# Performance work log

Hardware: AMD Instinct MI355X
Metric: run time of the kernel (lower is better)

Reference implementation:

```python
import jax, jax.numpy as jnp
import numpy as np

B, S, H = 1, 2048, 4096
NH, NKV, HD = 32, 8, 128
GROUP = 128
NEG = jnp.float32(-1e9)


def setup_inputs() -> dict:
    key = jax.random.key(0)
    ks = jax.random.split(key, 13)
    inp = {"hidden_states": jax.random.normal(ks[0], (B, S, H), dtype=jnp.float32)}

    def qparams(k1, k2, k3, out_dim, in_dim):
        qw = jax.random.randint(k1, (out_dim, in_dim), 0, 16, dtype=jnp.int32)
        sc = jax.random.uniform(k2, (out_dim, in_dim // GROUP), dtype=jnp.float32) * 0.02 + 0.001
        zp = jax.random.randint(k3, (out_dim, in_dim // GROUP), 0, 16, dtype=jnp.int32)
        return qw, sc, zp

    inp["q_qw"], inp["q_sc"], inp["q_zp"] = qparams(ks[1], ks[2], ks[3], NH * HD, H)
    inp["k_qw"], inp["k_sc"], inp["k_zp"] = qparams(ks[4], ks[5], ks[6], NKV * HD, H)
    inp["v_qw"], inp["v_sc"], inp["v_zp"] = qparams(ks[7], ks[8], ks[9], NKV * HD, H)
    inp["o_qw"], inp["o_sc"], inp["o_zp"] = qparams(ks[10], ks[11], ks[12], NH * HD, H)
    return inp


def dequant(qw, sc, zp):
    # W4A16 groupwise dequant: w = (q - zero_point) * scale, group along input dim
    out_dim, in_dim = qw.shape
    g = in_dim // sc.shape[1]
    w = (qw.reshape(out_dim, -1, g) - zp[:, :, None]).astype(jnp.float32) * sc[:, :, None]
    return w.reshape(out_dim, in_dim)


def reference(hidden_states, q_qw, q_sc, q_zp, k_qw, k_sc, k_zp,
              v_qw, v_sc, v_zp, o_qw, o_sc, o_zp):
    x = hidden_states  # [B, S, H]
    grp = NH // NKV  # GQA groups = 4

    q = jnp.einsum('bsh,oh->bso', x, dequant(q_qw, q_sc, q_zp))
    k = jnp.einsum('bsh,oh->bso', x, dequant(k_qw, k_sc, k_zp))
    v = jnp.einsum('bsh,oh->bso', x, dequant(v_qw, v_sc, v_zp))

    # [B, NKV, grp, S, HD] for q; [B, NKV, S, HD] for k, v (avoid repeat_kv materialization)
    q = q.reshape(B, S, NKV, grp, HD).transpose(0, 2, 3, 1, 4)
    k = k.reshape(B, S, NKV, HD).transpose(0, 2, 1, 3)
    v = v.reshape(B, S, NKV, HD).transpose(0, 2, 1, 3)

    scale = 1.0 / jnp.sqrt(jnp.float32(HD))
    scores = jnp.einsum('bngqd,bnkd->bngqk', q, k) * scale  # [B,NKV,grp,S,S]
    causal = jnp.tril(jnp.ones((S, S), dtype=bool))
    scores = jnp.where(causal[None, None, None], scores, NEG)
    probs = jax.nn.softmax(scores, axis=-1)
    attn = jnp.einsum('bngqk,bnkd->bngqd', probs, v)  # [B,NKV,grp,S,HD]

    attn = attn.transpose(0, 3, 1, 2, 4).reshape(B, S, NH * HD)
    out = jnp.einsum('bso,ho->bsh', attn, dequant(o_qw, o_sc, o_zp).T.T) if False else jnp.einsum('bsf,of->bso', attn, dequant(o_qw, o_sc, o_zp))
    return out
```

## Files before the change

### kernel.cpp

```cpp
#include <hip/hip_runtime.h>
#include <stdint.h>

#define DI __device__ __forceinline__

typedef __attribute__((ext_vector_type(8))) _Float16 f16x8;
typedef __attribute__((ext_vector_type(4))) float f32x4;
typedef __attribute__((ext_vector_type(4))) int   i32x4;
typedef __attribute__((ext_vector_type(4))) float fvec4;
typedef __attribute__((ext_vector_type(8))) unsigned short u16x8;
typedef __attribute__((ext_vector_type(4))) unsigned short u16x4;

constexpr int S2   = 2048;
constexpr int NHD  = 4096;
constexpr int KVD  = 1024;
constexpr int QKVW = 6144;
constexpr float SCALE_LOG2E = 0.08838834764831845f * 1.4426950408889634f;

DI unsigned short f32_f16(float f) {
    union { _Float16 h; unsigned short u; } v;
    v.h = (_Float16)f;
    return v.u;
}

DI f32x4 mfma16(f16x8 a, f16x8 b, f32x4 c) {
    return __builtin_amdgcn_mfma_f32_16x16x32_f16(a, b, c, 0, 0, 0);
}

DI void load_lds16(const void* g, void* l) {
    __builtin_amdgcn_global_load_lds(
        (const __attribute__((address_space(1))) void*)(uintptr_t)g,
        (__attribute__((address_space(3))) void*)(uintptr_t)l, 16, 0, 0);
}

DI void prep_body(const int* __restrict__ qw, const float* __restrict__ sc,
                  const int* __restrict__ zp, unsigned short* __restrict__ outW,
                  int blk, int tid) {
    long long t = (long long)blk * 256 + tid;
    long long base = t * 8;
    int n = (int)(base >> 12);
    int g = (int)((base >> 7) & 31);
    float s = sc[n * 32 + g];
    int   z = zp[n * 32 + g];
    i32x4 a = *(const i32x4*)(qw + base);
    i32x4 b = *(const i32x4*)(qw + base + 4);
    u16x8 o;
#pragma unroll
    for (int j = 0; j < 4; ++j) {
        o[j]     = f32_f16((float)(a[j] - z) * s);
        o[4 + j] = f32_f16((float)(b[j] - z) * s);
    }
    *(u16x8*)(outW + base) = o;
}

__global__ __launch_bounds__(256) void k_prep_all(
    const float* __restrict__ hs, unsigned short* __restrict__ x16,
    const int* __restrict__ qqw, const float* __restrict__ qsc, const int* __restrict__ qzp,
    const int* __restrict__ kqw, const float* __restrict__ ksc, const int* __restrict__ kzp,
    const int* __restrict__ vqw, const float* __restrict__ vsc, const int* __restrict__ vzp,
    unsigned short* __restrict__ wbuf) {
    const int b = blockIdx.x, tid = threadIdx.x;
    if (b < 8192) {
        int i = (b * 256 + tid) * 4;
        fvec4 v = *(const fvec4*)(hs + i);
        u16x4 o;
#pragma unroll
        for (int j = 0; j < 4; ++j) o[j] = f32_f16(v[j]);
        *(u16x4*)(x16 + i) = o;
    } else if (b < 16384) {
        prep_body(qqw, qsc, qzp, wbuf, b - 8192, tid);
    } else if (b < 18432) {
        prep_body(kqw, ksc, kzp, wbuf + (size_t)4096 * 4096, b - 16384, tid);
    } else {
        prep_body(vqw, vsc, vzp, wbuf + (size_t)5120 * 4096, b - 18432, tid);
    }
}

__global__ __launch_bounds__(256) void k_prep(const int* __restrict__ qw,
                                              const float* __restrict__ sc,
                                              const int* __restrict__ zp,
                                              unsigned short* __restrict__ outW) {
    prep_body(qw, sc, zp, outW, blockIdx.x, threadIdx.x);
}

template <typename CT, int NREP>
__global__ __launch_bounds__(512) void k_gemm8(const unsigned short* __restrict__ A,
                                               const unsigned short* __restrict__ B,
                                               CT* __restrict__ C, int N) {
    constexpr int K = 4096, BK = 32, NT = K / BK;
    constexpr int BN = NREP * 64;
    __shared__ __align__(16) unsigned short Al[3][256 * 32];
    __shared__ __align__(16) unsigned short Bl[3][BN * 32];
    const int nbx = N / BN;
    const int tot = nbx * (int)gridDim.y;
    const int hg  = (int)blockIdx.x + (int)blockIdx.y * nbx;
    const int lid = (hg & 7) * (tot >> 3) + (hg >> 3);
    const int m0 = (lid / nbx) * 256, n0 = (lid % nbx) * BN;
    const int tid = threadIdx.x;
    const int w = tid >> 6, lane = tid & 63;
    const int wm = w >> 2, wn = w & 3;
    const int lq = lane & 15, lg = lane >> 4;
    const int cx = (lg ^ ((lq >> 1) & 3)) << 3;
    const int srow = lane >> 2;
    const int gc = (((lane & 3) ^ ((lane >> 3) & 3)) << 3);
    f32x4 acc[8][NREP] = {};

    auto stage = [&](int k0, int sl) {
#pragma unroll
        for (int j = 0; j < 2; ++j)
            load_lds16(A + (long long)(m0 + (j * 8 + w) * 16 + srow) * K + k0 + gc,
                       &Al[sl][(j * 8 + w) * 512]);
        if constexpr (NREP == 4) {
#pragma unroll
            for (int j = 0; j < 2; ++j)
                load_lds16(B + (long long)(n0 + (j * 8 + w) * 16 + srow) * K + k0 + gc,
                           &Bl[sl][(j * 8 + w) * 512]);
        } else if constexpr (NREP == 3) {
            if (w < 4) {
#pragma unroll
                for (int i = 0; i < 2; ++i) {
                    const int r0 = w * 32 + i * 16;
                    load_lds16(B + (long long)(n0 + r0 + srow) * K + k0 + gc,
                               &Bl[sl][r0 * 32]);
                }
            } else {
                const int r0 = 128 + (w - 4) * 16;
                load_lds16(B + (long long)(n0 + r0 + srow) * K + k0 + gc,
                           &Bl[sl][r0 * 32]);
            }
        } else {
            load_lds16(B + (long long)(n0 + w * 16 + srow) * K + k0 + gc,
                       &Bl[sl][w * 512]);
        }
    };

    stage(0, 0);
    stage(BK, 1);
    int cs = 0, ss = 2;
    for (int kt = 0; kt < NT; ++kt) {
        if (kt < NT - 1) {
            if constexpr (NREP == 3) {
                if (w < 4) asm volatile("s_waitcnt vmcnt(4)" ::: "memory");
                else       asm volatile("s_waitcnt vmcnt(3)" ::: "memory");
            } else if constexpr (NREP == 4) {
                asm volatile("s_waitcnt vmcnt(4)" ::: "memory");
            } else {
                asm volatile("s_waitcnt vmcnt(3)" ::: "memory");
            }
        } else {
            asm volatile("s_waitcnt vmcnt(0)" ::: "memory");
        }
        __builtin_amdgcn_s_barrier();
        __builtin_amdgcn_sched_barrier(0);
        if (kt + 2 < NT) stage((kt + 2) * BK, ss);
        f16x8 af[8], bf[NREP];
#pragma unroll
        for (int i = 0; i < 8; ++i)
            af[i] = *(const f16x8*)(&Al[cs][(wm * 128 + i * 16 + lq) * 32 + cx]);
#pragma unroll
        for (int i = 0; i < NREP; ++i)
            bf[i] = *(const f16x8*)(&Bl[cs][(wn * (NREP * 16) + i * 16 + lq) * 32 + cx]);
        __builtin_amdgcn_s_setprio(1);
#pragma unroll
        for (int mi = 0; mi < 8; ++mi)
#pragma unroll
            for (int ni = 0; ni < NREP; ++ni)
                acc[mi][ni] = mfma16(af[mi], bf[ni], acc[mi][ni]);
        __builtin_amdgcn_s_setprio(0);
        __builtin_amdgcn_sched_barrier(0);
        if (++cs == 3) cs = 0;
        if (++ss == 3) ss = 0;
    }
#pragma unroll
    for (int mi = 0; mi < 8; ++mi)
#pragma unroll
        for (int ni = 0; ni < NREP; ++ni)
#pragma unroll
            for (int r = 0; r < 4; ++r) {
                const int row = m0 + wm * 128 + mi * 16 + lg * 4 + r;
                const int col = n0 + wn * (NREP * 16) + ni * 16 + lq;
                const float v = acc[mi][ni][r];
                if constexpr (sizeof(CT) == 2) C[(long long)row * N + col] = (CT)f32_f16(v);
                else                           C[(long long)row * N + col] = v;
            }
}

template <typename CT>
__global__ __launch_bounds__(512) void k_gemm2(const unsigned short* __restrict__ A,
                                               const unsigned short* __restrict__ B,
                                               CT* __restrict__ C, int N) {
    constexpr int K = 4096, BK = 64, NT = K / BK;
    __shared__ __align__(16) unsigned short Al[3][128 * 64];
    __shared__ __align__(16) unsigned short Bl[3][256 * 64];
    const int nbx = N / 256;
    const int tot = nbx * (int)gridDim.y;
    const int hg  = (int)blockIdx.x + (int)blockIdx.y * nbx;
    const int lid = (hg & 7) * (tot >> 3) + (hg >> 3);
    const int m0 = (lid / nbx) * 128, n0 = (lid % nbx) * 256;
    const int tid = threadIdx.x;
    const int w = tid >> 6, lane = tid & 63;
    const int wm = w >> 2, wn = w & 3;
    const int lq = lane & 15, lg = lane >> 4;
    const int rsub = lane >> 3;
    const int gch  = ((lane & 7) ^ rsub) << 3;
    f32x4 acc[4][4] = {};

    auto stage = [&](int k0, int sl) {
#pragma unroll
        for (int i = 0; i < 2; ++i) {
            const int r0 = w * 16 + i * 8;
            load_lds16(A + (long long)(m0 + r0 + rsub) * K + k0 + gch, &Al[sl][r0 * 64]);
        }
#pragma unroll
        for (int i = 0; i < 4; ++i) {
            const int r0 = w * 32 + i * 8;
            load_lds16(B + (long long)(n0 + r0 + rsub) * K + k0 + gch, &Bl[sl][r0 * 64]);
        }
    };

    stage(0, 0);
    stage(BK, 1);
    int cs = 0, ss = 2;
    for (int kt = 0; kt < NT; ++kt) {
        if (kt < NT - 1) asm volatile("s_waitcnt vmcnt(6)" ::: "memory");
        else             asm volatile("s_waitcnt vmcnt(0)" ::: "memory");
        __builtin_amdgcn_s_barrier();
        __builtin_amdgcn_sched_barrier(0);
        if (kt + 2 < NT) stage((kt + 2) * BK, ss);
        f16x8 af[4][2], bf[4][2];
#pragma unroll
        for (int i = 0; i < 4; ++i)
#pragma unroll
            for (int kk = 0; kk < 2; ++kk) {
                const int ar = wm * 64 + i * 16 + lq;
                const int br = wn * 64 + i * 16 + lq;
                af[i][kk] = *(const f16x8*)(&Al[cs][ar * 64 + (((kk * 4 + lg) ^ (lq & 7)) << 3)]);
                bf[i][kk] = *(const f16x8*)(&Bl[cs][br * 64 + (((kk * 4 + lg) ^ (lq & 7)) << 3)]);
            }
        __builtin_amdgcn_s_setprio(1);
#pragma unroll
        for (int mi = 0; mi < 4; ++mi)
#pragma unroll
            for (int ni = 0; ni < 4; ++ni)
#pragma unroll
                for (int kk = 0; kk < 2; ++kk)
                    acc[mi][ni] = mfma16(af[mi][kk], bf[ni][kk], acc[mi][ni]);
        __builtin_amdgcn_s_setprio(0);
        __builtin_amdgcn_sched_barrier(0);
        if (++cs == 3) cs = 0;
        if (++ss == 3) ss = 0;
    }
#pragma unroll
    for (int mi = 0; mi < 4; ++mi)
#pragma unroll
        for (int ni = 0; ni < 4; ++ni)
#pragma unroll
            for (int r = 0; r < 4; ++r) {
                const int row = m0 + wm * 64 + mi * 16 + lg * 4 + r;
                const int col = n0 + wn * 64 + ni * 16 + lq;
                const float v = acc[mi][ni][r];
                if constexpr (sizeof(CT) == 2) C[(long long)row * N + col] = (CT)f32_f16(v);
                else                           C[(long long)row * N + col] = v;
            }
}

__global__ __launch_bounds__(256) void k_transpose_v(const unsigned short* __restrict__ QKV,
                                                     unsigned short* __restrict__ VT) {
    __shared__ unsigned short tile[32][33];
    const int s0 = blockIdx.x * 32, d0 = blockIdx.y * 32, hk = blockIdx.z;
    const int tx = threadIdx.x & 31, ty = threadIdx.x >> 5;
#pragma unroll
    for (int j = 0; j < 4; ++j)
        tile[ty + j * 8][tx] =
            QKV[(long long)(s0 + ty + j * 8) * QKVW + (NHD + KVD) + hk * 128 + d0 + tx];
    __syncthreads();
#pragma unroll
    for (int j = 0; j < 4; ++j)
        VT[((long long)hk * 128 + d0 + ty + j * 8) * S2 + s0 + tx] = tile[tx][ty + j * 8];
}

__global__ __launch_bounds__(256, 4) void k_attn(const unsigned short* __restrict__ QKV,
                                                 const unsigned short* __restrict__ VT,
                                                 unsigned short* __restrict__ O) {
    __shared__ __align__(16) unsigned short Ks[2][32 * 128];
    __shared__ __align__(16) unsigned short Vs[2][128 * 32];
    __shared__ __align__(16) unsigned short Ps[4][16 * 40];
    const int bid = blockIdx.x;
    const int hkv = bid & 7;
    const int tq  = bid >> 3;
    const int g   = (tq < 64) ? tq : 191 - tq;
    const int nt  = (g >> 1) + 1;
    const int q0  = g * 16;
    const int tid = threadIdx.x;
    const int w = tid >> 6, lane = tid & 63;
    const int lq = lane & 15, lg = lane >> 4;
    const int h = hkv * 4 + w;

    const unsigned short* Kg  = QKV + NHD + hkv * 128;
    const unsigned short* VTg = VT + (long long)hkv * 128 * S2;

    const int ksr = lane >> 4;
    const int ksc = lane & 15;
    const int vsr = lane >> 2;
    const int vsc = lane & 3;
    const int vsx = (lane >> 3) & 3;

    f16x8 qf[4];
    const unsigned short* qp = QKV + (long long)(q0 + lq) * QKVW + h * 128;
#pragma unroll
    for (int kc = 0; kc < 4; ++kc) qf[kc] = *(const f16x8*)(qp + kc * 32 + lg * 8);

    f32x4 oacc[8] = {};
    float m[4], l[4];
#pragma unroll
    for (int r = 0; r < 4; ++r) { m[r] = -1e30f; l[r] = 0.f; }

    auto stage = [&](int j0, int b) {
#pragma unroll
        for (int i = 0; i < 2; ++i) {
            const int r = 8 * w + 4 * i + ksr;
            load_lds16(Kg + (long long)(j0 + r) * QKVW + ((ksc ^ (r & 7)) << 3),
                       &Ks[b][(8 * w + 4 * i) * 128]);
        }
#pragma unroll
        for (int i = 0; i < 2; ++i) {
            const int r = 32 * w + 16 * i + vsr;
            load_lds16(VTg + (long long)r * S2 + j0 + ((vsc ^ vsx) << 3),
                       &Vs[b][(32 * w + 16 * i) * 32]);
        }
    };

    stage(0, 0);
    int buf = 0;
    for (int t = 0; t < nt; ++t) {
        const int j0 = t * 32;
        __syncthreads();
        if (t + 1 < nt) stage(j0 + 32, buf ^ 1);

        f32x4 sv[2] = {};
        __builtin_amdgcn_s_setprio(1);
#pragma unroll
        for (int kc = 0; kc < 4; ++kc)
#pragma unroll
            for (int jj = 0; jj < 2; ++jj) {
                const int c = (kc * 4 + lg) ^ (lq & 7);
                f16x8 kf = *(const f16x8*)&Ks[buf][(jj * 16 + lq) * 128 + c * 8];
                sv[jj] = mfma16(qf[kc], kf, sv[jj]);
            }
        __builtin_amdgcn_s_setprio(0);

        float t0a[4], t1a[4], pl[4];
        const bool diag = (t == nt - 1);
#pragma unroll
        for (int r = 0; r < 4; ++r) {
            float t0 = sv[0][r] * SCALE_LOG2E;
            float t1 = sv[1][r] * SCALE_LOG2E;
            if (diag) {
                const int qg = q0 + lg * 4 + r;
                if (j0 + lq > qg)      t0 = -INFINITY;
                if (j0 + 16 + lq > qg) t1 = -INFINITY;
            }
            t0a[r] = t0; t1a[r] = t1;
            pl[r] = fmaxf(t0, t1);
        }
        const bool grow = (pl[0] > m[0] + 8.f) || (pl[1] > m[1] + 8.f) ||
                          (pl[2] > m[2] + 8.f) || (pl[3] > m[3] + 8.f);
        if (__any(grow)) {
#pragma unroll
            for (int r = 0; r < 4; ++r) {
                float mx = pl[r];
                mx = fmaxf(mx, __shfl_xor(mx, 1));
                mx = fmaxf(mx, __shfl_xor(mx, 2));
                mx = fmaxf(mx, __shfl_xor(mx, 4));
                mx = fmaxf(mx, __shfl_xor(mx, 8));
                const float mn = fmaxf(m[r], mx);
                const float alpha = exp2f(m[r] - mn);
                m[r] = mn;
                l[r] *= alpha;
#pragma unroll
                for (int nb = 0; nb < 8; ++nb) oacc[nb][r] *= alpha;
            }
        }
#pragma unroll
        for (int r = 0; r < 4; ++r) {
            const float p0 = exp2f(t0a[r] - m[r]);
            const float p1 = exp2f(t1a[r] - m[r]);
            l[r] += p0 + p1;
            Ps[w][(lg * 4 + r) * 40 + lq]      = f32_f16(p0);
            Ps[w][(lg * 4 + r) * 40 + 16 + lq] = f32_f16(p1);
        }
        const f16x8 pf = *(const f16x8*)&Ps[w][lq * 40 + lg * 8];
        __builtin_amdgcn_s_setprio(1);
#pragma unroll
        for (int nb = 0; nb < 8; ++nb) {
            const int c = lg ^ ((lq >> 1) & 3);
            f16x8 vf = *(const f16x8*)&Vs[buf][(nb * 16 + lq) * 32 + c * 8];
            oacc[nb] = mfma16(pf, vf, oacc[nb]);
        }
        __builtin_amdgcn_s_setprio(0);
        buf ^= 1;
    }

    float linv[4];
#pragma unroll
    for (int r = 0; r < 4; ++r) {
        float s = l[r];
        s += __shfl_xor(s, 1);
        s += __shfl_xor(s, 2);
        s += __shfl_xor(s, 4);
        s += __shfl_xor(s, 8);
        linv[r] = 1.0f / s;
    }
#pragma unroll
    for (int nb = 0; nb < 8; ++nb)
#pragma unroll
        for (int r = 0; r < 4; ++r) {
            const int row = q0 + lg * 4 + r;
            const int col = h * 128 + nb * 16 + lq;
            O[(long long)row * NHD + col] = f32_f16(oacc[nb][r] * linv[r]);
        }
}

extern "C" void kernel_launch(void* const* d_in, const int* in_sizes, int n_in,
                              void* d_out, int out_size, void* d_ws, size_t ws_size,
                              hipStream_t stream) {
    (void)in_sizes; (void)n_in; (void)out_size; (void)ws_size;
    const float* hs  = (const float*)d_in[0];
    const int*   qqw = (const int*)d_in[1];
    const float* qsc = (const float*)d_in[2];
    const int*   qzp = (const int*)d_in[3];
    const int*   kqw = (const int*)d_in[4];
    const float* ksc = (const float*)d_in[5];
    const int*   kzp = (const int*)d_in[6];
    const int*   vqw = (const int*)d_in[7];
    const float* vsc = (const float*)d_in[8];
    const int*   vzp = (const int*)d_in[9];
    const int*   oqw = (const int*)d_in[10];
    const float* osc = (const float*)d_in[11];
    const int*   ozp = (const int*)d_in[12];

    char* ws = (char*)d_ws;
    unsigned short* x16  = (unsigned short*)(ws);
    unsigned short* wbuf = (unsigned short*)(ws + (16ULL << 20));
    unsigned short* vt   = (unsigned short*)(ws + (65ULL << 20));
    unsigned short* xatt = (unsigned short*)(ws + (69ULL << 20));
    unsigned short* qkv  = (unsigned short*)d_out;
    float* out = (float*)d_out;

    k_prep_all<<<20480, 256, 0, stream>>>(hs, x16, qqw, qsc, qzp,
                                          kqw, ksc, kzp, vqw, vsc, vzp, wbuf);
    k_gemm8<unsigned short, 3><<<dim3(32, 8), 512, 0, stream>>>(x16, wbuf, qkv, QKVW);
    k_transpose_v<<<dim3(64, 4, 8), 256, 0, stream>>>(qkv, vt);
    k_prep<<<8192, 256, 0, stream>>>(oqw, osc, ozp, wbuf);
    k_attn<<<1024, 256, 0, stream>>>(qkv, vt, xatt);
    k_gemm2<float><<<dim3(16, 16), 512, 0, stream>>>(xatt, wbuf, out, 4096);
}
```

Before: 304.9 us.

## Tile V transpose into per-block chunks and load V fragments directly from global

The V transpose kernel now writes V in 32-token tiled blocks of 128x32, so each attention step's V tile is contiguous. The attention kernel drops the LDS staging of V and has each wave load its V fragments straight from global/L2 into registers at the top of each iteration. Separately, the GEMM block-index mapping is changed to iterate over M first within a column of N tiles, altering L2 reuse order. This removes LDS traffic and shared memory for V but adds global load latency per iteration, and all four waves load the same V data redundantly.

After: 343.9 us. +12.8%, slower.

```diff
diff --git a/kernel.cpp b/kernel.cpp
--- a/kernel.cpp
+++ b/kernel.cpp
@@ -94,7 +94,8 @@
     const int tot = nbx * (int)gridDim.y;
     const int hg  = (int)blockIdx.x + (int)blockIdx.y * nbx;
     const int lid = (hg & 7) * (tot >> 3) + (hg >> 3);
-    const int m0 = (lid / nbx) * 256, n0 = (lid % nbx) * BN;
+    const int m0 = (lid % (int)gridDim.y) * 256;
+    const int n0 = (lid / (int)gridDim.y) * BN;
     const int tid = threadIdx.x;
     const int w = tid >> 6, lane = tid & 63;
     const int wm = w >> 2, wn = w & 3;
@@ -195,7 +196,8 @@
     const int tot = nbx * (int)gridDim.y;
     const int hg  = (int)blockIdx.x + (int)blockIdx.y * nbx;
     const int lid = (hg & 7) * (tot >> 3) + (hg >> 3);
-    const int m0 = (lid / nbx) * 128, n0 = (lid % nbx) * 256;
+    const int m0 = (lid % (int)gridDim.y) * 128;
+    const int n0 = (lid / (int)gridDim.y) * 256;
     const int tid = threadIdx.x;
     const int w = tid >> 6, lane = tid & 63;
     const int wm = w >> 2, wn = w & 3;
@@ -275,14 +277,14 @@
     __syncthreads();
 #pragma unroll
     for (int j = 0; j < 4; ++j)
-        VT[((long long)hk * 128 + d0 + ty + j * 8) * S2 + s0 + tx] = tile[tx][ty + j * 8];
+        VT[(((long long)hk * 64 + (s0 >> 5)) * 128 + d0 + ty + j * 8) * 32 + tx] =
+            tile[tx][ty + j * 8];
 }
 
 __global__ __launch_bounds__(256, 4) void k_attn(const unsigned short* __restrict__ QKV,
                                                  const unsigned short* __restrict__ VT,
                                                  unsigned short* __restrict__ O) {
     __shared__ __align__(16) unsigned short Ks[2][32 * 128];
-    __shared__ __align__(16) unsigned short Vs[2][128 * 32];
     __shared__ __align__(16) unsigned short Ps[4][16 * 40];
     const int bid = blockIdx.x;
     const int hkv = bid & 7;
@@ -296,13 +298,10 @@
     const int h = hkv * 4 + w;
 
     const unsigned short* Kg  = QKV + NHD + hkv * 128;
-    const unsigned short* VTg = VT + (long long)hkv * 128 * S2;
+    const unsigned short* VTg = VT + (long long)hkv * (64 * 128 * 32);
 
     const int ksr = lane >> 4;
     const int ksc = lane & 15;
-    const int vsr = lane >> 2;
-    const int vsc = lane & 3;
-    const int vsx = (lane >> 3) & 3;
 
     f16x8 qf[4];
     const unsigned short* qp = QKV + (long long)(q0 + lq) * QKVW + h * 128;
@@ -320,12 +319,6 @@
             const int r = 8 * w + 4 * i + ksr;
             load_lds16(Kg + (long long)(j0 + r) * QKVW + ((ksc ^ (r & 7)) << 3),
                        &Ks[b][(8 * w + 4 * i) * 128]);
-        }
-#pragma unroll
-        for (int i = 0; i < 2; ++i) {
-            const int r = 32 * w + 16 * i + vsr;
-            load_lds16(VTg + (long long)r * S2 + j0 + ((vsc ^ vsx) << 3),
-                       &Vs[b][(32 * w + 16 * i) * 32]);
         }
     };
 
@@ -335,6 +328,12 @@
         const int j0 = t * 32;
         __syncthreads();
         if (t + 1 < nt) stage(j0 + 32, buf ^ 1);
+
+        f16x8 vf[8];
+        const unsigned short* vtp = VTg + (long long)t * (128 * 32);
+#pragma unroll
+        for (int nb = 0; nb < 8; ++nb)
+            vf[nb] = *(const f16x8*)(vtp + (nb * 16 + lq) * 32 + lg * 8);
 
         f32x4 sv[2] = {};
         __builtin_amdgcn_s_setprio(1);
@@ -391,11 +390,8 @@
         const f16x8 pf = *(const f16x8*)&Ps[w][lq * 40 + lg * 8];
         __builtin_amdgcn_s_setprio(1);
 #pragma unroll
-        for (int nb = 0; nb < 8; ++nb) {
-            const int c = lg ^ ((lq >> 1) & 3);
-            f16x8 vf = *(const f16x8*)&Vs[buf][(nb * 16 + lq) * 32 + c * 8];
-            oacc[nb] = mfma16(pf, vf, oacc[nb]);
-        }
+        for (int nb = 0; nb < 8; ++nb)
+            oacc[nb] = mfma16(pf, vf[nb], oacc[nb]);
         __builtin_amdgcn_s_setprio(0);
         buf ^= 1;
     }
```
